# Kernel tuning notes

Hardware: AMD Instinct MI355X
Metric: run time of the kernel (lower is better)

The kernel has to match this reference:

```python
import jax, jax.numpy as jnp
import numpy as np

B, N, F = 32, 2048, 32  # batch, num_elements, feature_size = num_classes + num_geometry


def setup_inputs() -> dict:
    key = jax.random.key(0)
    ks = jax.random.split(key, 5)
    s = 1.0 / np.sqrt(F)
    return {
        "x": jax.random.normal(ks[0], (B, N, F), dtype=jnp.float32),
        "w_psi": jax.random.normal(ks[1], (F, F), dtype=jnp.float32) * s,
        "b_psi": jnp.zeros((F,), dtype=jnp.float32),
        "w_phi": jax.random.normal(ks[2], (F, F), dtype=jnp.float32) * s,
        "b_phi": jnp.zeros((F,), dtype=jnp.float32),
        "w_u": jax.random.normal(ks[3], (F, F), dtype=jnp.float32) * s,
        "b_u": jnp.zeros((F,), dtype=jnp.float32),
        "w_r": jax.random.normal(ks[4], (F, F), dtype=jnp.float32) * s,
    }


def reference(x, w_psi, b_psi, w_phi, b_phi, w_u, b_u, w_r):
    # psi/phi: per-element linear embeddings; u: relu unary representation
    psi = x @ w_psi + b_psi                      # [B,N,F]
    phi = x @ w_phi + b_phi                      # [B,N,F]
    u = jax.nn.relu(x @ w_u + b_u)               # [B,N,F]
    # H(i,j) = psi_i . phi_j  -> all-pairs scalar affinities
    scores = jnp.einsum('bif,bjf->bij', psi, phi)          # [B,N,N]
    # sum_j H(i,j) * u_j, then remove the j==i self term
    att = jnp.einsum('bij,bjf->bif', scores, u)            # [B,N,F]
    diag = jnp.einsum('bif,bif->bi', psi, phi)             # H(i,i)
    att = att - diag[..., None] * u
    # residual: W_r * (attention / N) + f_i
    return (att / N) @ w_r + x
```

## Files before the change

kernel.cpp:

```cpp
#include <hip/hip_runtime.h>


namespace {
constexpr int kF = 32;
constexpr int kN = 2048;
constexpr int kB = 32;
}

typedef __attribute__((ext_vector_type(8))) short bf16x8;
typedef __attribute__((ext_vector_type(16))) float f32x16;

union BF8 { bf16x8 v; int i[4]; };

__device__ inline unsigned short f2bf(float f) {
    union { float f; unsigned int u; } c; c.f = f;
    unsigned int r = c.u + 0x7FFFu + ((c.u >> 16) & 1u);
    return (unsigned short)(r >> 16);
}
__device__ inline int pk2(float lo, float hi) {
    return (int)f2bf(lo) | ((int)f2bf(hi) << 16);
}

__device__ inline void load_wfrags(const float* __restrict__ W, int col, int h,
                                   bf16x8& f0, bf16x8& f1) {
    BF8 a, b;
#pragma unroll
    for (int q = 0; q < 4; ++q)
        a.i[q] = pk2(W[(8 * h + 2 * q) * kF + col], W[(8 * h + 2 * q + 1) * kF + col]);
#pragma unroll
    for (int q = 0; q < 4; ++q)
        b.i[q] = pk2(W[(16 + 8 * h + 2 * q) * kF + col], W[(16 + 8 * h + 2 * q + 1) * kF + col]);
    f0 = a.v; f1 = b.v;
}

__device__ inline void load_xfrags(const float* __restrict__ xr, int h,
                                   bf16x8& f0, bf16x8& f1) {
    float4 a = *(const float4*)(xr + 8 * h);
    float4 b = *(const float4*)(xr + 8 * h + 4);
    float4 c = *(const float4*)(xr + 16 + 8 * h);
    float4 d = *(const float4*)(xr + 16 + 8 * h + 4);
    BF8 u0, u1;
    u0.i[0] = pk2(a.x, a.y); u0.i[1] = pk2(a.z, a.w);
    u0.i[2] = pk2(b.x, b.y); u0.i[3] = pk2(b.z, b.w);
    u1.i[0] = pk2(c.x, c.y); u1.i[1] = pk2(c.z, c.w);
    u1.i[2] = pk2(d.x, d.y); u1.i[3] = pk2(d.z, d.w);
    f0 = u0.v; f1 = u1.v;
}

__device__ inline void c_to_kfrags(const f32x16& v, int h, bf16x8& f0, bf16x8& f1) {
    int p[8], t[8];
#pragma unroll
    for (int q = 0; q < 8; ++q) p[q] = pk2(v[2 * q], v[2 * q + 1]);
#pragma unroll
    for (int q = 0; q < 8; ++q) t[q] = __shfl_xor(p[q], 32, 64);
    BF8 a, b;
    a.i[0] = h ? t[2] : p[0];
    a.i[1] = h ? t[3] : p[1];
    a.i[2] = h ? p[2] : t[0];
    a.i[3] = h ? p[3] : t[1];
    b.i[0] = h ? t[6] : p[4];
    b.i[1] = h ? t[7] : p[5];
    b.i[2] = h ? p[6] : t[4];
    b.i[3] = h ? p[7] : t[5];
    f0 = a.v; f1 = b.v;
}

__device__ inline f32x16 zero16() {
    f32x16 z;
#pragma unroll
    for (int i = 0; i < 16; ++i) z[i] = 0.f;
    return z;
}

#define MFMA(A, B, C) __builtin_amdgcn_mfma_f32_32x32x16_bf16(A, B, C, 0, 0, 0)

__global__ __launch_bounds__(256, 2) void k_partial_m(
    const float* __restrict__ x,
    const float* __restrict__ w_phi, const float* __restrict__ b_phi,
    const float* __restrict__ w_u,   const float* __restrict__ b_u,
    float* __restrict__ m_out)
{
    __shared__ float red_s[4][64 * 20];

    const int tid = threadIdx.x;
    const int lane = tid & 63;
    const int w = tid >> 6;
    const int col = lane & 31;
    const int h = lane >> 5;

    const int row0 = blockIdx.x * 128 + w * 32;
    const int b = row0 >> 11;

    bf16x8 ax0, ax1;
    load_xfrags(x + (size_t)(row0 + col) * kF, h, ax0, ax1);
    bf16x8 bp0, bp1, bu0, bu1;
    load_wfrags(w_phi, col, h, bp0, bp1);
    load_wfrags(w_u,   col, h, bu0, bu1);

    f32x16 phiC = zero16(), uC = zero16();
    phiC = MFMA(ax0, bp0, phiC); phiC = MFMA(ax1, bp1, phiC);
    uC   = MFMA(ax0, bu0, uC);   uC   = MFMA(ax1, bu1, uC);

    const float bphi = b_phi[col];
    const float bu = b_u[col];
#pragma unroll
    for (int r = 0; r < 16; ++r) {
        phiC[r] += bphi;
        uC[r] = fmaxf(uC[r] + bu, 0.f);
    }

    bf16x8 ap0, ap1, bfu0, bfu1;
    c_to_kfrags(phiC, h, ap0, ap1);
    c_to_kfrags(uC, h, bfu0, bfu1);
    f32x16 macc = zero16();
    macc = MFMA(ap0, bfu0, macc);
    macc = MFMA(ap1, bfu1, macc);

    float* rs = red_s[w] + lane * 20;
#pragma unroll
    for (int q = 0; q < 4; ++q) {
        float4 v = make_float4(macc[4 * q], macc[4 * q + 1], macc[4 * q + 2], macc[4 * q + 3]);
        *(float4*)(rs + 4 * q) = v;
    }
    __syncthreads();

    const int lp = tid >> 2;
    const int q = tid & 3;
    float4 s = make_float4(0.f, 0.f, 0.f, 0.f);
#pragma unroll
    for (int ww = 0; ww < 4; ++ww) {
        float4 v = *(const float4*)(red_s[ww] + lp * 20 + 4 * q);
        s.x += v.x; s.y += v.y; s.z += v.z; s.w += v.w;
    }
    const int g = lp & 31;
    const int hp = lp >> 5;
    const int f0 = 8 * q + 4 * hp;
    float* mdst = m_out + (size_t)b * kF * kF + (size_t)f0 * kF + g;
    atomicAdd(mdst,            s.x);
    atomicAdd(mdst + kF,       s.y);
    atomicAdd(mdst + 2 * kF,   s.z);
    atomicAdd(mdst + 3 * kF,   s.w);
}

__global__ __launch_bounds__(256, 2) void k_relation(
    const float* __restrict__ x,
    const float* __restrict__ w_psi, const float* __restrict__ b_psi,
    const float* __restrict__ w_phi, const float* __restrict__ b_phi,
    const float* __restrict__ w_u,   const float* __restrict__ b_u,
    const float* __restrict__ w_r,
    const float* __restrict__ m_in,
    float* __restrict__ out)
{
    __shared__ float t_s[4][32 * 36];

    const int tid = threadIdx.x;
    const int lane = tid & 63;
    const int w = tid >> 6;
    const int col = lane & 31;
    const int h = lane >> 5;

    const int row0 = blockIdx.x * 128 + w * 32;
    const int b = row0 >> 11;
    const float* __restrict__ m_b = m_in + (size_t)b * kF * kF;

    bf16x8 bx0, bx1;
    load_xfrags(x + (size_t)(row0 + col) * kF, h, bx0, bx1);

    bf16x8 aps0, aps1, aph0, aph1, au0, au1;
    load_wfrags(w_psi, col, h, aps0, aps1);
    load_wfrags(w_phi, col, h, aph0, aph1);
    load_wfrags(w_u,   col, h, au0, au1);

    f32x16 psiT = zero16(), phiT = zero16(), uT = zero16();
    psiT = MFMA(aps0, bx0, psiT); psiT = MFMA(aps1, bx1, psiT);
    phiT = MFMA(aph0, bx0, phiT); phiT = MFMA(aph1, bx1, phiT);
    uT   = MFMA(au0,  bx0, uT);   uT   = MFMA(au1,  bx1, uT);

#pragma unroll
    for (int r = 0; r < 16; ++r) {
        const int g = (r & 3) + 8 * (r >> 2);
        psiT[r] += h ? b_psi[g + 4] : b_psi[g];
        phiT[r] += h ? b_phi[g + 4] : b_phi[g];
        uT[r] = fmaxf(uT[r] + (h ? b_u[g + 4] : b_u[g]), 0.f);
    }

    float d = 0.f;
#pragma unroll
    for (int r = 0; r < 16; ++r) d += psiT[r] * phiT[r];
    d += __shfl_xor(d, 32, 64);

    bf16x8 am0, am1, bps0, bps1;
    load_wfrags(m_b, col, h, am0, am1);
    c_to_kfrags(psiT, h, bps0, bps1);
    f32x16 attT = zero16();
    attT = MFMA(am0, bps0, attT);
    attT = MFMA(am1, bps1, attT);

    const float inv_n = 1.0f / (float)kN;
#pragma unroll
    for (int r = 0; r < 16; ++r) attT[r] = (attT[r] - d * uT[r]) * inv_n;

    bf16x8 ar0, ar1, bt0, bt1;
    load_wfrags(w_r, col, h, ar0, ar1);
    c_to_kfrags(attT, h, bt0, bt1);
    f32x16 corrT = zero16();
    corrT = MFMA(ar0, bt0, corrT);
    corrT = MFMA(ar1, bt1, corrT);

    float* ts = t_s[w];
#pragma unroll
    for (int q = 0; q < 4; ++q) {
        float4 v = make_float4(corrT[4 * q], corrT[4 * q + 1], corrT[4 * q + 2], corrT[4 * q + 3]);
        *(float4*)(ts + col * 36 + 8 * q + 4 * h) = v;
    }
    const size_t gbase = (size_t)row0 * kF;
#pragma unroll
    for (int q = 0; q < 4; ++q) {
        const int idx = q * 256 + lane * 4;
        const int el = idx >> 5;
        const int c = idx & 31;
        float4 cv = *(const float4*)(ts + el * 36 + c);
        float4 xv = *(const float4*)(x + gbase + idx);
        float4 o = make_float4(xv.x + cv.x, xv.y + cv.y, xv.z + cv.z, xv.w + cv.w);
        *(float4*)(out + gbase + idx) = o;
    }
}

extern "C" void kernel_launch(void* const* d_in, const int* in_sizes, int n_in,
                              void* d_out, int out_size, void* d_ws, size_t ws_size,
                              hipStream_t stream) {
    const float* x     = (const float*)d_in[0];
    const float* w_psi = (const float*)d_in[1];
    const float* b_psi = (const float*)d_in[2];
    const float* w_phi = (const float*)d_in[3];
    const float* b_phi = (const float*)d_in[4];
    const float* w_u   = (const float*)d_in[5];
    const float* b_u   = (const float*)d_in[6];
    const float* w_r   = (const float*)d_in[7];
    float* out = (float*)d_out;
    float* m_ws = (float*)d_ws;

    hipMemsetAsync(d_ws, 0, (size_t)kB * kF * kF * sizeof(float), stream);

    k_partial_m<<<dim3(512), 256, 0, stream>>>(x, w_phi, b_phi, w_u, b_u, m_ws);
    k_relation<<<dim3(512), 256, 0, stream>>>(x, w_psi, b_psi, w_phi, b_phi,
                                              w_u, b_u, w_r, m_ws, out);
}
```

Before: 83.34 us.

## Replace atomic M accumulation with per-block partials reduced in relation kernel

The first kernel now writes each block's 32x32 partial of phi^T·u to a workspace slot with plain stores, replacing the global atomicAdds. The relation kernel sums the 16 partials for its batch into shared memory before use. This removes the memset launch and atomic contention. In exchange, every relation block redundantly reads 16 KB of partials and waits at an extra barrier. The w_r fragment load is also hoisted earlier.

```diff
diff --git a/kernel.cpp b/kernel.cpp
--- a/kernel.cpp
+++ b/kernel.cpp
@@ -21,15 +21,15 @@
     return (int)f2bf(lo) | ((int)f2bf(hi) << 16);
 }
 
-__device__ inline void load_wfrags(const float* __restrict__ W, int col, int h,
+__device__ inline void load_wfrags(const float* __restrict__ W, int ld, int col, int h,
                                    bf16x8& f0, bf16x8& f1) {
     BF8 a, b;
 #pragma unroll
     for (int q = 0; q < 4; ++q)
-        a.i[q] = pk2(W[(8 * h + 2 * q) * kF + col], W[(8 * h + 2 * q + 1) * kF + col]);
+        a.i[q] = pk2(W[(8 * h + 2 * q) * ld + col], W[(8 * h + 2 * q + 1) * ld + col]);
 #pragma unroll
     for (int q = 0; q < 4; ++q)
-        b.i[q] = pk2(W[(16 + 8 * h + 2 * q) * kF + col], W[(16 + 8 * h + 2 * q + 1) * kF + col]);
+        b.i[q] = pk2(W[(16 + 8 * h + 2 * q) * ld + col], W[(16 + 8 * h + 2 * q + 1) * ld + col]);
     f0 = a.v; f1 = b.v;
 }
 
@@ -78,7 +78,7 @@
     const float* __restrict__ x,
     const float* __restrict__ w_phi, const float* __restrict__ b_phi,
     const float* __restrict__ w_u,   const float* __restrict__ b_u,
-    float* __restrict__ m_out)
+    float* __restrict__ part)
 {
     __shared__ float red_s[4][64 * 20];
 
@@ -87,15 +87,14 @@
     const int w = tid >> 6;
     const int col = lane & 31;
     const int h = lane >> 5;
-
-    const int row0 = blockIdx.x * 128 + w * 32;
-    const int b = row0 >> 11;
+    const int blk = blockIdx.x;
+    const int row0 = blk * 128 + w * 32;
 
     bf16x8 ax0, ax1;
     load_xfrags(x + (size_t)(row0 + col) * kF, h, ax0, ax1);
     bf16x8 bp0, bp1, bu0, bu1;
-    load_wfrags(w_phi, col, h, bp0, bp1);
-    load_wfrags(w_u,   col, h, bu0, bu1);
+    load_wfrags(w_phi, kF, col, h, bp0, bp1);
+    load_wfrags(w_u,   kF, col, h, bu0, bu1);
 
     f32x16 phiC = zero16(), uC = zero16();
     phiC = MFMA(ax0, bp0, phiC); phiC = MFMA(ax1, bp1, phiC);
@@ -109,19 +108,18 @@
         uC[r] = fmaxf(uC[r] + bu, 0.f);
     }
 
-    bf16x8 ap0, ap1, bfu0, bfu1;
+    bf16x8 ap0, ap1, fu0, fu1;
     c_to_kfrags(phiC, h, ap0, ap1);
-    c_to_kfrags(uC, h, bfu0, bfu1);
+    c_to_kfrags(uC, h, fu0, fu1);
     f32x16 macc = zero16();
-    macc = MFMA(ap0, bfu0, macc);
-    macc = MFMA(ap1, bfu1, macc);
+    macc = MFMA(ap0, fu0, macc);
+    macc = MFMA(ap1, fu1, macc);
 
     float* rs = red_s[w] + lane * 20;
 #pragma unroll
-    for (int q = 0; q < 4; ++q) {
-        float4 v = make_float4(macc[4 * q], macc[4 * q + 1], macc[4 * q + 2], macc[4 * q + 3]);
-        *(float4*)(rs + 4 * q) = v;
-    }
+    for (int q = 0; q < 4; ++q)
+        *(float4*)(rs + 4 * q) = make_float4(macc[4 * q], macc[4 * q + 1],
+                                             macc[4 * q + 2], macc[4 * q + 3]);
     __syncthreads();
 
     const int lp = tid >> 2;
@@ -132,14 +130,7 @@
         float4 v = *(const float4*)(red_s[ww] + lp * 20 + 4 * q);
         s.x += v.x; s.y += v.y; s.z += v.z; s.w += v.w;
     }
-    const int g = lp & 31;
-    const int hp = lp >> 5;
-    const int f0 = 8 * q + 4 * hp;
-    float* mdst = m_out + (size_t)b * kF * kF + (size_t)f0 * kF + g;
-    atomicAdd(mdst,            s.x);
-    atomicAdd(mdst + kF,       s.y);
-    atomicAdd(mdst + 2 * kF,   s.z);
-    atomicAdd(mdst + 3 * kF,   s.w);
+    *(float4*)(part + (size_t)blk * 1024 + tid * 4) = s;
 }
 
 __global__ __launch_bounds__(256, 2) void k_relation(
@@ -148,40 +139,59 @@
     const float* __restrict__ w_phi, const float* __restrict__ b_phi,
     const float* __restrict__ w_u,   const float* __restrict__ b_u,
     const float* __restrict__ w_r,
-    const float* __restrict__ m_in,
+    const float* __restrict__ part,
     float* __restrict__ out)
 {
     __shared__ float t_s[4][32 * 36];
+    __shared__ float m_s[kF * 33];
 
     const int tid = threadIdx.x;
     const int lane = tid & 63;
     const int w = tid >> 6;
     const int col = lane & 31;
     const int h = lane >> 5;
-
-    const int row0 = blockIdx.x * 128 + w * 32;
-    const int b = row0 >> 11;
-    const float* __restrict__ m_b = m_in + (size_t)b * kF * kF;
-
-    bf16x8 bx0, bx1;
-    load_xfrags(x + (size_t)(row0 + col) * kF, h, bx0, bx1);
-
-    bf16x8 aps0, aps1, aph0, aph1, au0, au1;
-    load_wfrags(w_psi, col, h, aps0, aps1);
-    load_wfrags(w_phi, col, h, aph0, aph1);
-    load_wfrags(w_u,   col, h, au0, au1);
+    const int blk = blockIdx.x;
+    const int row0 = blk * 128 + w * 32;
+    const int b = blk >> 4;
+
+    const float* pb = part + (size_t)(b * 16) * 1024 + tid * 4;
+    float4 ms = make_float4(0.f, 0.f, 0.f, 0.f);
+#pragma unroll
+    for (int p = 0; p < 16; ++p) {
+        float4 v = *(const float4*)(pb + p * 1024);
+        ms.x += v.x; ms.y += v.y; ms.z += v.z; ms.w += v.w;
+    }
+    {
+        const int lp = tid >> 2;
+        const int q = tid & 3;
+        const int g = lp & 31;
+        const int hp = lp >> 5;
+        const int f0 = 8 * q + 4 * hp;
+        m_s[(f0 + 0) * 33 + g] = ms.x;
+        m_s[(f0 + 1) * 33 + g] = ms.y;
+        m_s[(f0 + 2) * 33 + g] = ms.z;
+        m_s[(f0 + 3) * 33 + g] = ms.w;
+    }
+
+    bf16x8 ax0, ax1;
+    load_xfrags(x + (size_t)(row0 + col) * kF, h, ax0, ax1);
+    bf16x8 aps0, aps1, aph0, aph1, au0, au1, ar0, ar1;
+    load_wfrags(w_psi, kF, col, h, aps0, aps1);
+    load_wfrags(w_phi, kF, col, h, aph0, aph1);
+    load_wfrags(w_u,   kF, col, h, au0, au1);
+    load_wfrags(w_r,   kF, col, h, ar0, ar1);
 
     f32x16 psiT = zero16(), phiT = zero16(), uT = zero16();
-    psiT = MFMA(aps0, bx0, psiT); psiT = MFMA(aps1, bx1, psiT);
-    phiT = MFMA(aph0, bx0, phiT); phiT = MFMA(aph1, bx1, phiT);
-    uT   = MFMA(au0,  bx0, uT);   uT   = MFMA(au1,  bx1, uT);
+    psiT = MFMA(aps0, ax0, psiT); psiT = MFMA(aps1, ax1, psiT);
+    phiT = MFMA(aph0, ax0, phiT); phiT = MFMA(aph1, ax1, phiT);
+    uT   = MFMA(au0,  ax0, uT);   uT   = MFMA(au1,  ax1, uT);
 
 #pragma unroll
     for (int r = 0; r < 16; ++r) {
-        const int g = (r & 3) + 8 * (r >> 2);
-        psiT[r] += h ? b_psi[g + 4] : b_psi[g];
-        phiT[r] += h ? b_phi[g + 4] : b_phi[g];
-        uT[r] = fmaxf(uT[r] + (h ? b_u[g + 4] : b_u[g]), 0.f);
+        const int gg = (r & 3) + 8 * (r >> 2);
+        psiT[r] += h ? b_psi[gg + 4] : b_psi[gg];
+        phiT[r] += h ? b_phi[gg + 4] : b_phi[gg];
+        uT[r] = fmaxf(uT[r] + (h ? b_u[gg + 4] : b_u[gg]), 0.f);
     }
 
     float d = 0.f;
@@ -189,8 +199,11 @@
     for (int r = 0; r < 16; ++r) d += psiT[r] * phiT[r];
     d += __shfl_xor(d, 32, 64);
 
-    bf16x8 am0, am1, bps0, bps1;
-    load_wfrags(m_b, col, h, am0, am1);
+    __syncthreads();
+    bf16x8 am0, am1;
+    load_wfrags(m_s, 33, col, h, am0, am1);
+
+    bf16x8 bps0, bps1;
     c_to_kfrags(psiT, h, bps0, bps1);
     f32x16 attT = zero16();
     attT = MFMA(am0, bps0, attT);
@@ -200,8 +213,7 @@
 #pragma unroll
     for (int r = 0; r < 16; ++r) attT[r] = (attT[r] - d * uT[r]) * inv_n;
 
-    bf16x8 ar0, ar1, bt0, bt1;
-    load_wfrags(w_r, col, h, ar0, ar1);
+    bf16x8 bt0, bt1;
     c_to_kfrags(attT, h, bt0, bt1);
     f32x16 corrT = zero16();
     corrT = MFMA(ar0, bt0, corrT);
@@ -209,20 +221,21 @@
 
     float* ts = t_s[w];
 #pragma unroll
-    for (int q = 0; q < 4; ++q) {
-        float4 v = make_float4(corrT[4 * q], corrT[4 * q + 1], corrT[4 * q + 2], corrT[4 * q + 3]);
-        *(float4*)(ts + col * 36 + 8 * q + 4 * h) = v;
-    }
+    for (int qq = 0; qq < 4; ++qq)
+        *(float4*)(ts + col * 36 + 8 * qq + 4 * h) =
+            make_float4(corrT[4 * qq], corrT[4 * qq + 1],
+                        corrT[4 * qq + 2], corrT[4 * qq + 3]);
+
     const size_t gbase = (size_t)row0 * kF;
 #pragma unroll
-    for (int q = 0; q < 4; ++q) {
-        const int idx = q * 256 + lane * 4;
+    for (int qq = 0; qq < 4; ++qq) {
+        const int idx = qq * 256 + lane * 4;
         const int el = idx >> 5;
-        const int c = idx & 31;
-        float4 cv = *(const float4*)(ts + el * 36 + c);
+        const int cc = idx & 31;
+        float4 cv = *(const float4*)(ts + el * 36 + cc);
         float4 xv = *(const float4*)(x + gbase + idx);
-        float4 o = make_float4(xv.x + cv.x, xv.y + cv.y, xv.z + cv.z, xv.w + cv.w);
-        *(float4*)(out + gbase + idx) = o;
+        *(float4*)(out + gbase + idx) =
+            make_float4(xv.x + cv.x, xv.y + cv.y, xv.z + cv.z, xv.w + cv.w);
     }
 }
 
@@ -238,11 +251,9 @@
     const float* b_u   = (const float*)d_in[6];
     const float* w_r   = (const float*)d_in[7];
     float* out = (float*)d_out;
-    float* m_ws = (float*)d_ws;
-
-    hipMemsetAsync(d_ws, 0, (size_t)kB * kF * kF * sizeof(float), stream);
-
-    k_partial_m<<<dim3(512), 256, 0, stream>>>(x, w_phi, b_phi, w_u, b_u, m_ws);
+    float* part = (float*)d_ws;
+
+    k_partial_m<<<dim3(512), 256, 0, stream>>>(x, w_phi, b_phi, w_u, b_u, part);
     k_relation<<<dim3(512), 256, 0, stream>>>(x, w_psi, b_psi, w_phi, b_phi,
-                                              w_u, b_u, w_r, m_ws, out);
-}
+                                              w_u, b_u, w_r, part, out);
+}
```

Result: no change. 84.19 us (+1.0%).
